# Optimization experiments

Hardware: AMD Instinct MI355X
Metric: run time of the kernel (lower is better)

The kernel has to match this reference:

```python
import jax, jax.numpy as jnp
import numpy as np

B, C, L = 32, 128, 4096          # batch, n_channels, signal length
P, Q = 100, 20                   # n_projections, n_quantiles


def setup_inputs() -> dict:
    key = jax.random.key(0)
    k1, k2, k3, k4 = jax.random.split(key, 4)
    X = jax.random.normal(k1, (B, C, L), dtype=jnp.float32)
    # conv1d kernel of shape (P, C, 1) collapsed to (P, C)
    W = jax.random.normal(k2, (P, C), dtype=jnp.float32)
    s = 2.33 * jnp.sqrt(jnp.float32(C))
    min_vals = -s + 0.1 * jax.random.normal(k3, (P,), dtype=jnp.float32)
    max_vals = s + 0.1 * jax.random.normal(k4, (P,), dtype=jnp.float32)
    return {"X": X, "W": W, "min_vals": min_vals, "max_vals": max_vals}


def reference(X, W, min_vals, max_vals):
    # kernel-size-1 conv1d == channel projection
    a = jnp.einsum('bcl,pc->bpl', X, W)  # [B, P, L]
    fracs = jnp.arange(1, Q + 1, dtype=a.dtype) / jnp.asarray(Q + 1, a.dtype)
    thr = min_vals[None, :] + (max_vals - min_vals)[None, :] * fracs[:, None]  # [Q, P]

    def body(carry, t):  # t: [P] thresholds for one quantile
        cdf_q = jnp.mean((a < t[None, :, None]).astype(a.dtype), axis=-1)  # [B, P]
        return carry, cdf_q

    _, cdf = jax.lax.scan(body, None, thr)          # [Q, B, P]
    cdf = jnp.transpose(cdf, (1, 2, 0))             # [B, P, Q]
    return cdf.reshape(B, P * Q)
```

## Files before the change

kernel.cpp:

```cpp
#include <hip/hip_runtime.h>
#include <hip/hip_bf16.h>

#define B_   32
#define C_   128
#define L_   4096
#define P_   100
#define NPT  7
#define Q_   20
#define NBIN 21
#define NCH  (NPT * 4)
#define CHS  512

typedef short          bf16x8 __attribute__((ext_vector_type(8)));
typedef float          f32x4  __attribute__((ext_vector_type(4)));
typedef unsigned short u16x8  __attribute__((ext_vector_type(8)));

__device__ inline unsigned short f2bf(float f) {
    __hip_bfloat16 h = __float2bfloat16(f);
    unsigned short u; __builtin_memcpy(&u, &h, 2);
    return u;
}

__global__ void prep_w_kernel(const float* __restrict__ W, unsigned short* __restrict__ Wf) {
    const int t = blockIdx.x * 256 + threadIdx.x;
    if (t >= NCH * 64) return;
    const int chunk = t >> 6, lane = t & 63;
    const int pt = chunk >> 2, ks = chunk & 3;
    const int p  = pt * 16 + (lane & 15);
    const int c0 = ks * 32 + (lane >> 4) * 8;
    u16x8 v;
#pragma unroll
    for (int j = 0; j < 8; ++j)
        v[j] = (p < P_) ? f2bf(W[p * C_ + c0 + j]) : (unsigned short)0;
    *(u16x8*)(Wf + (size_t)t * 8) = v;
}

__global__ __launch_bounds__(256, 4)
void radon_mfma3_kernel(const float* __restrict__ X, const unsigned short* __restrict__ Wf,
                        const float* __restrict__ minv, const float* __restrict__ maxv,
                        float* __restrict__ out) {
    __shared__ unsigned short Wlds[NCH * CHS];
    __shared__ int   hist[P_ * NBIN];
    __shared__ float mn_s[P_], invd_s[P_];

    const int tid  = threadIdx.x;
    const int b    = blockIdx.y;
    const int lblk = blockIdx.x;
    const int wave = tid >> 6;
    const int lane = tid & 63;
    const int quad = lane >> 4;
    const int nn   = lane & 15;

    {
        const int4* src = (const int4*)Wf;
        int4* dst = (int4*)Wlds;
#pragma unroll
        for (int k = 0; k < NCH * 64 / 256; ++k)
            dst[tid + k * 256] = src[tid + k * 256];
    }
    for (int i = tid; i < P_; i += 256) {
        const float mn = minv[i];
        mn_s[i]   = mn;
        invd_s[i] = (float)NBIN / (maxv[i] - mn);
    }
    for (int i = tid; i < P_ * NBIN; i += 256) hist[i] = 0;
    __syncthreads();

    const int l0 = lblk * 128 + wave * 32;
    const float* Xb = X + (size_t)b * C_ * L_;
    float xv[2][4][8];
#pragma unroll
    for (int lt = 0; lt < 2; ++lt)
#pragma unroll
        for (int ks = 0; ks < 4; ++ks)
#pragma unroll
            for (int j = 0; j < 8; ++j)
                xv[lt][ks][j] = Xb[(size_t)(ks * 32 + quad * 8 + j) * L_ + l0 + lt * 16 + nn];

    bf16x8 bfrag[2][4];
#pragma unroll
    for (int lt = 0; lt < 2; ++lt)
#pragma unroll
        for (int ks = 0; ks < 4; ++ks) {
            unsigned int u[4];
#pragma unroll
            for (int jp = 0; jp < 4; ++jp) {
                __hip_bfloat162 h2 = __float22bfloat162_rn(
                    make_float2(xv[lt][ks][2 * jp], xv[lt][ks][2 * jp + 1]));
                __builtin_memcpy(&u[jp], &h2, 4);
            }
            __builtin_memcpy(&bfrag[lt][ks], u, 16);
        }

    for (int pt = 0; pt < NPT; ++pt) {
        bf16x8 afrag[4];
#pragma unroll
        for (int ks = 0; ks < 4; ++ks)
            afrag[ks] = *(const bf16x8*)(&Wlds[((pt * 4 + ks) * 64 + lane) * 8]);

        f32x4 acc0 = {0.f, 0.f, 0.f, 0.f};
        f32x4 acc1 = {0.f, 0.f, 0.f, 0.f};
#pragma unroll
        for (int ks = 0; ks < 4; ++ks) {
            acc0 = __builtin_amdgcn_mfma_f32_16x16x32_bf16(afrag[ks], bfrag[0][ks], acc0, 0, 0, 0);
            acc1 = __builtin_amdgcn_mfma_f32_16x16x32_bf16(afrag[ks], bfrag[1][ks], acc1, 0, 0, 0);
        }

#pragma unroll
        for (int r = 0; r < 4; ++r) {
            const int p = pt * 16 + quad * 4 + r;
            if (p < P_) {
                const float mn = mn_s[p], invd = invd_s[p];
                {
                    const float t = (acc0[r] - mn) * invd;
                    int k = 0;
                    if (t > 0.f) { const int ki = (int)t; k = (ki > 20) ? 20 : ki; }
                    atomicAdd(&hist[p * NBIN + k], 1);
                }
                {
                    const float t = (acc1[r] - mn) * invd;
                    int k = 0;
                    if (t > 0.f) { const int ki = (int)t; k = (ki > 20) ? 20 : ki; }
                    atomicAdd(&hist[p * NBIN + k], 1);
                }
            }
        }
    }
    __syncthreads();

    for (int i = tid; i < P_ * Q_; i += 256) {
        const int p  = i / Q_;
        const int qi = i - p * Q_;
        int s = 0;
        for (int k = 0; k <= qi; ++k) s += hist[p * NBIN + k];
        atomicAdd(&out[((size_t)b * P_ + p) * Q_ + qi], (float)s * (1.0f / (float)L_));
    }
}

extern "C" void kernel_launch(void* const* d_in, const int* in_sizes, int n_in,
                              void* d_out, int out_size, void* d_ws, size_t ws_size,
                              hipStream_t stream) {
    const float* X  = (const float*)d_in[0];
    const float* W  = (const float*)d_in[1];
    const float* mn = (const float*)d_in[2];
    const float* mx = (const float*)d_in[3];
    float* out = (float*)d_out;
    unsigned short* Wf = (unsigned short*)d_ws;

    hipMemsetAsync(out, 0, (size_t)out_size * sizeof(float), stream);
    prep_w_kernel<<<NCH * 64 / 256, 256, 0, stream>>>(W, Wf);

    dim3 grid(L_ / 128, B_);
    radon_mfma3_kernel<<<grid, dim3(256), 0, stream>>>(X, Wf, mn, mx, out);
}
```

Before: 108.5 us.

## Write per-block histograms to workspace and reduce in a separate kernel

The main kernel no longer does a prefix sum and float atomicAdd into the output at the end. Each block now stores its raw integer histogram to workspace, and a new reduce kernel sums the 32 partial histograms per batch and writes the cumulative output directly. This removes the output memset and the global atomic contention. Threshold parameters are precomputed once into device globals by a small kernel, so each block no longer recomputes them in LDS. The cost is two extra launches and a workspace round trip of roughly 8 KB per block.

```diff
diff --git a/kernel.cpp b/kernel.cpp
--- a/kernel.cpp
+++ b/kernel.cpp
@@ -10,10 +10,16 @@
 #define NBIN 21
 #define NCH  (NPT * 4)
 #define CHS  512
+#define NLB  32
+#define HSZ  (P_ * NBIN)
+#define WS_HIST_OFF 32768
 
 typedef short          bf16x8 __attribute__((ext_vector_type(8)));
 typedef float          f32x4  __attribute__((ext_vector_type(4)));
 typedef unsigned short u16x8  __attribute__((ext_vector_type(8)));
+
+__device__ float mn_c[P_];
+__device__ float invd_c[P_];
 
 __device__ inline unsigned short f2bf(float f) {
     __hip_bfloat16 h = __float2bfloat16(f);
@@ -35,13 +41,20 @@
     *(u16x8*)(Wf + (size_t)t * 8) = v;
 }
 
+__global__ void prep_thr_kernel(const float* __restrict__ minv, const float* __restrict__ maxv) {
+    const int p = threadIdx.x;
+    if (p < P_) {
+        const float mn = minv[p];
+        mn_c[p]   = mn;
+        invd_c[p] = (float)NBIN / (maxv[p] - mn);
+    }
+}
+
 __global__ __launch_bounds__(256, 4)
-void radon_mfma3_kernel(const float* __restrict__ X, const unsigned short* __restrict__ Wf,
-                        const float* __restrict__ minv, const float* __restrict__ maxv,
-                        float* __restrict__ out) {
+void radon_mfma4_kernel(const float* __restrict__ X, const unsigned short* __restrict__ Wf,
+                        int* __restrict__ hist_out) {
     __shared__ unsigned short Wlds[NCH * CHS];
-    __shared__ int   hist[P_ * NBIN];
-    __shared__ float mn_s[P_], invd_s[P_];
+    __shared__ int hist[HSZ];
 
     const int tid  = threadIdx.x;
     const int b    = blockIdx.y;
@@ -58,12 +71,7 @@
         for (int k = 0; k < NCH * 64 / 256; ++k)
             dst[tid + k * 256] = src[tid + k * 256];
     }
-    for (int i = tid; i < P_; i += 256) {
-        const float mn = minv[i];
-        mn_s[i]   = mn;
-        invd_s[i] = (float)NBIN / (maxv[i] - mn);
-    }
-    for (int i = tid; i < P_ * NBIN; i += 256) hist[i] = 0;
+    for (int i = tid; i < HSZ; i += 256) hist[i] = 0;
     __syncthreads();
 
     const int l0 = lblk * 128 + wave * 32;
@@ -110,7 +118,8 @@
         for (int r = 0; r < 4; ++r) {
             const int p = pt * 16 + quad * 4 + r;
             if (p < P_) {
-                const float mn = mn_s[p], invd = invd_s[p];
+                const float mn   = mn_c[p];
+                const float invd = invd_c[p];
                 {
                     const float t = (acc0[r] - mn) * invd;
                     int k = 0;
@@ -128,12 +137,30 @@
     }
     __syncthreads();
 
-    for (int i = tid; i < P_ * Q_; i += 256) {
-        const int p  = i / Q_;
-        const int qi = i - p * Q_;
-        int s = 0;
-        for (int k = 0; k <= qi; ++k) s += hist[p * NBIN + k];
-        atomicAdd(&out[((size_t)b * P_ + p) * Q_ + qi], (float)s * (1.0f / (float)L_));
+    int* dst = hist_out + (size_t)(b * NLB + lblk) * HSZ;
+    for (int i = tid; i < HSZ; i += 256) dst[i] = hist[i];
+}
+
+__global__ __launch_bounds__(128)
+void reduce_kernel(const int* __restrict__ hist_in, float* __restrict__ out) {
+    const int b = blockIdx.x;
+    const int p = threadIdx.x;
+    if (p >= P_) return;
+    int acc[NBIN];
+#pragma unroll
+    for (int k = 0; k < NBIN; ++k) acc[k] = 0;
+    const int* base = hist_in + (size_t)b * NLB * HSZ + p * NBIN;
+    for (int lb = 0; lb < NLB; ++lb) {
+        const int* h = base + (size_t)lb * HSZ;
+#pragma unroll
+        for (int k = 0; k < NBIN; ++k) acc[k] += h[k];
+    }
+    float* o = out + ((size_t)b * P_ + p) * Q_;
+    int s = 0;
+#pragma unroll
+    for (int qi = 0; qi < Q_; ++qi) {
+        s += acc[qi];
+        o[qi] = (float)s * (1.0f / (float)L_);
     }
 }
 
@@ -146,10 +173,13 @@
     const float* mx = (const float*)d_in[3];
     float* out = (float*)d_out;
     unsigned short* Wf = (unsigned short*)d_ws;
+    int* hist_ws = (int*)((char*)d_ws + WS_HIST_OFF);
 
-    hipMemsetAsync(out, 0, (size_t)out_size * sizeof(float), stream);
     prep_w_kernel<<<NCH * 64 / 256, 256, 0, stream>>>(W, Wf);
+    prep_thr_kernel<<<1, 128, 0, stream>>>(mn, mx);
 
-    dim3 grid(L_ / 128, B_);
-    radon_mfma3_kernel<<<grid, dim3(256), 0, stream>>>(X, Wf, mn, mx, out);
+    dim3 grid(NLB, B_);
+    radon_mfma4_kernel<<<grid, dim3(256), 0, stream>>>(X, Wf, hist_ws);
+
+    reduce_kernel<<<B_, 128, 0, stream>>>(hist_ws, out);
 }
```

Result: slower. 116.0 us (+6.9%).

## Stage X tile into LDS via direct global-to-LDS DMA, read W from global

Applied to the files above, without the earlier changes.

The X tile (128 channels by 128 positions) is now loaded with global_load_lds straight into shared memory, replacing per-thread strided global loads. Fragments are then built from LDS. The W fragments are read directly from global or cache instead of being staged in LDS, and the min/inv-range tables move into device globals computed by the prep kernel. LDS use grows to about 64KB plus the histogram, so occupancy drops to 2 blocks per CU, and W reads now take the global-memory path inside the inner loop.

```diff
diff --git a/kernel.cpp b/kernel.cpp
--- a/kernel.cpp
+++ b/kernel.cpp
@@ -9,11 +9,14 @@
 #define Q_   20
 #define NBIN 21
 #define NCH  (NPT * 4)
-#define CHS  512
+#define HSZ  (P_ * NBIN)
 
 typedef short          bf16x8 __attribute__((ext_vector_type(8)));
 typedef float          f32x4  __attribute__((ext_vector_type(4)));
 typedef unsigned short u16x8  __attribute__((ext_vector_type(8)));
+
+__device__ float mn_c[P_];
+__device__ float invd_c[P_];
 
 __device__ inline unsigned short f2bf(float f) {
     __hip_bfloat16 h = __float2bfloat16(f);
@@ -21,27 +24,32 @@
     return u;
 }
 
-__global__ void prep_w_kernel(const float* __restrict__ W, unsigned short* __restrict__ Wf) {
+__global__ void prep_kernel(const float* __restrict__ W, const float* __restrict__ minv,
+                            const float* __restrict__ maxv, unsigned short* __restrict__ Wf) {
     const int t = blockIdx.x * 256 + threadIdx.x;
-    if (t >= NCH * 64) return;
-    const int chunk = t >> 6, lane = t & 63;
-    const int pt = chunk >> 2, ks = chunk & 3;
-    const int p  = pt * 16 + (lane & 15);
-    const int c0 = ks * 32 + (lane >> 4) * 8;
-    u16x8 v;
+    if (t < NCH * 64) {
+        const int chunk = t >> 6, lane = t & 63;
+        const int pt = chunk >> 2, ks = chunk & 3;
+        const int p  = pt * 16 + (lane & 15);
+        const int c0 = ks * 32 + (lane >> 4) * 8;
+        u16x8 v;
 #pragma unroll
-    for (int j = 0; j < 8; ++j)
-        v[j] = (p < P_) ? f2bf(W[p * C_ + c0 + j]) : (unsigned short)0;
-    *(u16x8*)(Wf + (size_t)t * 8) = v;
+        for (int j = 0; j < 8; ++j)
+            v[j] = (p < P_) ? f2bf(W[p * C_ + c0 + j]) : (unsigned short)0;
+        *(u16x8*)(Wf + (size_t)t * 8) = v;
+    } else if (t >= NCH * 64 && t < NCH * 64 + P_) {
+        const int p = t - NCH * 64;
+        const float mn = minv[p];
+        mn_c[p]   = mn;
+        invd_c[p] = (float)NBIN / (maxv[p] - mn);
+    }
 }
 
-__global__ __launch_bounds__(256, 4)
-void radon_mfma3_kernel(const float* __restrict__ X, const unsigned short* __restrict__ Wf,
-                        const float* __restrict__ minv, const float* __restrict__ maxv,
-                        float* __restrict__ out) {
-    __shared__ unsigned short Wlds[NCH * CHS];
-    __shared__ int   hist[P_ * NBIN];
-    __shared__ float mn_s[P_], invd_s[P_];
+__global__ __launch_bounds__(256, 2)
+void radon_dma_kernel(const float* __restrict__ X, const unsigned short* __restrict__ Wf,
+                      float* __restrict__ out) {
+    __shared__ float Xlds[C_ * 128];
+    __shared__ int   hist[HSZ];
 
     const int tid  = threadIdx.x;
     const int b    = blockIdx.y;
@@ -52,51 +60,45 @@
     const int nn   = lane & 15;
 
     {
-        const int4* src = (const int4*)Wf;
-        int4* dst = (int4*)Wlds;
+        const float* gb = X + ((size_t)b * C_ + (lane >> 5)) * L_ + lblk * 128 + (lane & 31) * 4;
 #pragma unroll
-        for (int k = 0; k < NCH * 64 / 256; ++k)
-            dst[tid + k * 256] = src[tid + k * 256];
+        for (int i = 0; i < 16; ++i) {
+            const int c0 = wave * 32 + i * 2;
+            __builtin_amdgcn_global_load_lds(
+                (const __attribute__((address_space(1))) unsigned int*)(gb + (size_t)c0 * L_),
+                (__attribute__((address_space(3))) unsigned int*)&Xlds[c0 * 128],
+                16, 0, 0);
+        }
     }
-    for (int i = tid; i < P_; i += 256) {
-        const float mn = minv[i];
-        mn_s[i]   = mn;
-        invd_s[i] = (float)NBIN / (maxv[i] - mn);
-    }
-    for (int i = tid; i < P_ * NBIN; i += 256) hist[i] = 0;
+    for (int i = tid; i < HSZ; i += 256) hist[i] = 0;
     __syncthreads();
-
-    const int l0 = lblk * 128 + wave * 32;
-    const float* Xb = X + (size_t)b * C_ * L_;
-    float xv[2][4][8];
-#pragma unroll
-    for (int lt = 0; lt < 2; ++lt)
-#pragma unroll
-        for (int ks = 0; ks < 4; ++ks)
-#pragma unroll
-            for (int j = 0; j < 8; ++j)
-                xv[lt][ks][j] = Xb[(size_t)(ks * 32 + quad * 8 + j) * L_ + l0 + lt * 16 + nn];
 
     bf16x8 bfrag[2][4];
 #pragma unroll
-    for (int lt = 0; lt < 2; ++lt)
+    for (int lt = 0; lt < 2; ++lt) {
+        const int ll = wave * 32 + lt * 16 + nn;
 #pragma unroll
         for (int ks = 0; ks < 4; ++ks) {
+            float xf[8];
+#pragma unroll
+            for (int j = 0; j < 8; ++j)
+                xf[j] = Xlds[(ks * 32 + quad * 8 + j) * 128 + ll];
             unsigned int u[4];
 #pragma unroll
             for (int jp = 0; jp < 4; ++jp) {
                 __hip_bfloat162 h2 = __float22bfloat162_rn(
-                    make_float2(xv[lt][ks][2 * jp], xv[lt][ks][2 * jp + 1]));
+                    make_float2(xf[2 * jp], xf[2 * jp + 1]));
                 __builtin_memcpy(&u[jp], &h2, 4);
             }
             __builtin_memcpy(&bfrag[lt][ks], u, 16);
         }
+    }
 
     for (int pt = 0; pt < NPT; ++pt) {
         bf16x8 afrag[4];
 #pragma unroll
         for (int ks = 0; ks < 4; ++ks)
-            afrag[ks] = *(const bf16x8*)(&Wlds[((pt * 4 + ks) * 64 + lane) * 8]);
+            afrag[ks] = *(const bf16x8*)(Wf + ((size_t)(pt * 4 + ks) * 64 + lane) * 8);
 
         f32x4 acc0 = {0.f, 0.f, 0.f, 0.f};
         f32x4 acc1 = {0.f, 0.f, 0.f, 0.f};
@@ -110,7 +112,8 @@
         for (int r = 0; r < 4; ++r) {
             const int p = pt * 16 + quad * 4 + r;
             if (p < P_) {
-                const float mn = mn_s[p], invd = invd_s[p];
+                const float mn   = mn_c[p];
+                const float invd = invd_c[p];
                 {
                     const float t = (acc0[r] - mn) * invd;
                     int k = 0;
@@ -148,8 +151,8 @@
     unsigned short* Wf = (unsigned short*)d_ws;
 
     hipMemsetAsync(out, 0, (size_t)out_size * sizeof(float), stream);
-    prep_w_kernel<<<NCH * 64 / 256, 256, 0, stream>>>(W, Wf);
+    prep_kernel<<<8, 256, 0, stream>>>(W, mn, mx, Wf);
 
     dim3 grid(L_ / 128, B_);
-    radon_mfma3_kernel<<<grid, dim3(256), 0, stream>>>(X, Wf, mn, mx, out);
+    radon_dma_kernel<<<grid, dim3(256), 0, stream>>>(X, Wf, out);
 }
```

New measurement: 119.3 us. 10.0% more time.
